# Kernel optimization log

Hardware: AMD Instinct MI355X
Metric: run time of the kernel (lower is better)

Reference implementation:

```python
import jax, jax.numpy as jnp
import numpy as np

N_NODES = 100000
N_EDGES = 1600000
D_IN = 256
D_OUT = 256


def _init_linear(key, out_f, in_f):
    # torch nn.Linear default: U(-1/sqrt(in_f), 1/sqrt(in_f))
    kw, kb = jax.random.split(key)
    bound = 1.0 / np.sqrt(in_f)
    W = jax.random.uniform(kw, (out_f, in_f), jnp.float32, -bound, bound)
    b = jax.random.uniform(kb, (out_f,), jnp.float32, -bound, bound)
    return W, b


def setup_inputs() -> dict:
    key = jax.random.key(0)
    ks = jax.random.split(key, 7)
    x = jax.random.normal(ks[0], (N_NODES, D_IN), jnp.float32)
    edge_index = jax.random.randint(ks[1], (2, N_EDGES), 0, N_NODES, jnp.int64)
    W1, b1 = _init_linear(ks[2], D_OUT, D_IN)
    W2, b2 = _init_linear(ks[3], D_OUT // 2, D_OUT)
    W3, b3 = _init_linear(ks[4], D_OUT // 2, D_OUT)
    Wd1, bd1 = _init_linear(ks[5], D_OUT, D_OUT)
    Wd2, bd2 = _init_linear(ks[6], 1, D_OUT)
    return {"x": x, "edge_index": edge_index,
            "W1": W1, "b1": b1, "W2": W2, "b2": b2, "W3": W3, "b3": b3,
            "Wd1": Wd1, "bd1": bd1, "Wd2": Wd2, "bd2": bd2}


def _l2norm(x):
    return x / jnp.linalg.norm(x, axis=-1, keepdims=True)


def reference(x, edge_index, W1, b1, W2, b2, W3, b3, Wd1, bd1, Wd2, bd2):
    src, dst = edge_index[0], edge_index[1]  # source_to_target flow
    x = jax.nn.relu(x @ W1.T + b1)           # [N, D_OUT]
    x = _l2norm(x)
    for _ in range(2):
        # sum-aggregate neighbor messages: scatter-add x[src] into dst
        nm = jax.ops.segment_sum(x[src], dst, num_segments=N_NODES)  # [N, D_OUT]
        x = jax.nn.relu(jnp.concatenate([x @ W2.T + b2, nm @ W3.T + b3], axis=-1))
        x = _l2norm(x)
    x = jax.nn.relu(x @ Wd1.T + bd1)
    return x @ Wd2.T + bd2                    # [N, 1]
```

## Files before the change

kernel.cpp:

```cpp
#include <hip/hip_runtime.h>
#include <math.h>


typedef _Float16 f16x8 __attribute__((ext_vector_type(8)));
typedef float    f32x16 __attribute__((ext_vector_type(16)));

constexpr int DIM = 256;
constexpr int BM  = 128;
constexpr int BK  = 32;
constexpr int SA  = 40;

__device__ __forceinline__ unsigned pk_hi2(float a, float b) {
    unsigned short ha = __builtin_bit_cast(unsigned short, (_Float16)a);
    unsigned short hb = __builtin_bit_cast(unsigned short, (_Float16)b);
    return (unsigned)ha | ((unsigned)hb << 16);
}
__device__ __forceinline__ unsigned pk_lo2(float a, float b) {
    _Float16 ha = (_Float16)a, hb = (_Float16)b;
    unsigned short la = __builtin_bit_cast(unsigned short, (_Float16)(a - (float)ha));
    unsigned short lb = __builtin_bit_cast(unsigned short, (_Float16)(b - (float)hb));
    return (unsigned)la | ((unsigned)lb << 16);
}
__device__ __forceinline__ unsigned pack_pair(float v) {
    _Float16 hi = (_Float16)v;
    _Float16 lo = (_Float16)(v - (float)hi);
    return (unsigned)__builtin_bit_cast(unsigned short, hi)
         | ((unsigned)__builtin_bit_cast(unsigned short, lo) << 16);
}

template <int AMODE, int EPI>
__device__ __forceinline__
void gemm_body(const void* __restrict__ Av,
               const float* __restrict__ WA, const float* __restrict__ WB,
               const float* __restrict__ bA, const float* __restrict__ bB,
               void* __restrict__ outv,
               const float* __restrict__ wd2, const float* __restrict__ bd2,
               float* __restrict__ out1, int M)
{
    __shared__ __align__(16) _Float16 smem[30720];
    _Float16* As_hi = smem;
    _Float16* As_lo = smem + 5120;
    _Float16* Ws_hi = smem + 10240;
    _Float16* Ws_lo = smem + 20480;

    const int tid = threadIdx.x;
    const int l31 = tid & 31;
    const int lh  = (tid >> 5) & 1;
    const int w   = tid >> 6;
    const int wr  = w >> 2;
    const int wc  = w & 3;
    const int bm0 = blockIdx.x * BM;

    const unsigned* Au = (const unsigned*)Av;
    const int srow = tid >> 2;
    const int sch  = (tid & 3) * 8;
    const int srw  = tid >> 1;
    const int scw  = (tid & 1) * 16;

    uint4 pa[2];
    auto fetchA = [&](int t) {
        const int k0 = t * BK;
        const int gr = bm0 + srow;
        if (gr < M) {
            pa[0] = *(const uint4*)&Au[(size_t)gr * 256 + k0 + sch];
            pa[1] = *(const uint4*)&Au[(size_t)gr * 256 + k0 + sch + 4];
        } else {
            pa[0] = uint4{0u,0u,0u,0u}; pa[1] = uint4{0u,0u,0u,0u};
        }
    };
    auto stageA = [&]() {
        uint4 hi, lo;
        if (AMODE == 0) {
            const float x0 = __builtin_bit_cast(float, pa[0].x);
            const float x1 = __builtin_bit_cast(float, pa[0].y);
            const float x2 = __builtin_bit_cast(float, pa[0].z);
            const float x3 = __builtin_bit_cast(float, pa[0].w);
            const float x4 = __builtin_bit_cast(float, pa[1].x);
            const float x5 = __builtin_bit_cast(float, pa[1].y);
            const float x6 = __builtin_bit_cast(float, pa[1].z);
            const float x7 = __builtin_bit_cast(float, pa[1].w);
            hi = uint4{pk_hi2(x0,x1), pk_hi2(x2,x3), pk_hi2(x4,x5), pk_hi2(x6,x7)};
            lo = uint4{pk_lo2(x0,x1), pk_lo2(x2,x3), pk_lo2(x4,x5), pk_lo2(x6,x7)};
        } else {
            hi = uint4{__builtin_amdgcn_perm(pa[0].y, pa[0].x, 0x05040100u),
                       __builtin_amdgcn_perm(pa[0].w, pa[0].z, 0x05040100u),
                       __builtin_amdgcn_perm(pa[1].y, pa[1].x, 0x05040100u),
                       __builtin_amdgcn_perm(pa[1].w, pa[1].z, 0x05040100u)};
            lo = uint4{__builtin_amdgcn_perm(pa[0].y, pa[0].x, 0x07060302u),
                       __builtin_amdgcn_perm(pa[0].w, pa[0].z, 0x07060302u),
                       __builtin_amdgcn_perm(pa[1].y, pa[1].x, 0x07060302u),
                       __builtin_amdgcn_perm(pa[1].w, pa[1].z, 0x07060302u)};
        }
        *(uint4*)&As_hi[srow * SA + sch] = hi;
        *(uint4*)&As_lo[srow * SA + sch] = lo;
    };
    auto stageW = [&](int t) {
        const int k0 = t * BK;
        const float* src = (srw < 128) ? &WA[(size_t)srw * 256]
                                       : &WB[(size_t)(srw - 128) * 256];
        const float4 w0 = *(const float4*)&src[k0 + scw];
        const float4 w1 = *(const float4*)&src[k0 + scw + 4];
        const float4 w2 = *(const float4*)&src[k0 + scw + 8];
        const float4 w3 = *(const float4*)&src[k0 + scw + 12];
        uint4 hi0{pk_hi2(w0.x,w0.y), pk_hi2(w0.z,w0.w), pk_hi2(w1.x,w1.y), pk_hi2(w1.z,w1.w)};
        uint4 hi1{pk_hi2(w2.x,w2.y), pk_hi2(w2.z,w2.w), pk_hi2(w3.x,w3.y), pk_hi2(w3.z,w3.w)};
        uint4 lo0{pk_lo2(w0.x,w0.y), pk_lo2(w0.z,w0.w), pk_lo2(w1.x,w1.y), pk_lo2(w1.z,w1.w)};
        uint4 lo1{pk_lo2(w2.x,w2.y), pk_lo2(w2.z,w2.w), pk_lo2(w3.x,w3.y), pk_lo2(w3.z,w3.w)};
        *(uint4*)&Ws_hi[srw * SA + scw]     = hi0;
        *(uint4*)&Ws_hi[srw * SA + scw + 8] = hi1;
        *(uint4*)&Ws_lo[srw * SA + scw]     = lo0;
        *(uint4*)&Ws_lo[srw * SA + scw + 8] = lo1;
    };

    f32x16 acc[2][2];
    #pragma unroll
    for (int tr = 0; tr < 2; ++tr)
        #pragma unroll
        for (int tc = 0; tc < 2; ++tc)
            #pragma unroll
            for (int i = 0; i < 16; ++i) acc[tr][tc][i] = 0.0f;

    fetchA(0);

    #pragma unroll 1
    for (int t = 0; t < DIM / BK; ++t) {
        stageA();
        stageW(t);
        __syncthreads();
        if (t < DIM / BK - 1) fetchA(t + 1);

        #pragma unroll
        for (int ks = 0; ks < 2; ++ks) {
            f16x8 ah[2], al[2], wh[2], wl[2];
            #pragma unroll
            for (int tr = 0; tr < 2; ++tr) {
                const int off = (wr * 64 + tr * 32 + l31) * SA + ks * 16 + lh * 8;
                ah[tr] = *(const f16x8*)&As_hi[off];
                al[tr] = *(const f16x8*)&As_lo[off];
            }
            #pragma unroll
            for (int tc = 0; tc < 2; ++tc) {
                const int off = (wc * 64 + tc * 32 + l31) * SA + ks * 16 + lh * 8;
                wh[tc] = *(const f16x8*)&Ws_hi[off];
                wl[tc] = *(const f16x8*)&Ws_lo[off];
            }
            #pragma unroll
            for (int tr = 0; tr < 2; ++tr)
                #pragma unroll
                for (int tc = 0; tc < 2; ++tc) {
                    acc[tr][tc] = __builtin_amdgcn_mfma_f32_32x32x16_f16(ah[tr], wh[tc], acc[tr][tc], 0, 0, 0);
                    acc[tr][tc] = __builtin_amdgcn_mfma_f32_32x32x16_f16(ah[tr], wl[tc], acc[tr][tc], 0, 0, 0);
                    acc[tr][tc] = __builtin_amdgcn_mfma_f32_32x32x16_f16(al[tr], wh[tc], acc[tr][tc], 0, 0, 0);
                }
        }
        __syncthreads();
    }


    if (EPI == 0) {
        float* z = (float*)outv;
        #pragma unroll
        for (int tr = 0; tr < 2; ++tr)
            #pragma unroll
            for (int i = 0; i < 16; ++i) {
                const int r  = wr * 64 + tr * 32 + 4 * lh + (i & 3) + 8 * (i >> 2);
                const int gr = bm0 + r;
                if (gr < M) {
                    #pragma unroll
                    for (int tc = 0; tc < 2; ++tc)
                        z[(size_t)gr * 256 + wc * 64 + tc * 32 + l31] = acc[tr][tc][i];
                }
            }
        return;
    }

    {
        float bias[2];
        #pragma unroll
        for (int tc = 0; tc < 2; ++tc) {
            const int col = wc * 64 + tc * 32 + l31;
            bias[tc] = (col < 128) ? bA[col] : bB[col - 128];
        }
        #pragma unroll
        for (int tr = 0; tr < 2; ++tr)
            #pragma unroll
            for (int tc = 0; tc < 2; ++tc)
                #pragma unroll
                for (int i = 0; i < 16; ++i)
                    acc[tr][tc][i] = fmaxf(acc[tr][tc][i] + bias[tc], 0.0f);
    }

    float* red = (float*)smem;

    if (EPI == 1) {
        #pragma unroll
        for (int tr = 0; tr < 2; ++tr)
            #pragma unroll
            for (int i = 0; i < 16; ++i) {
                float s = acc[tr][0][i] * acc[tr][0][i] + acc[tr][1][i] * acc[tr][1][i];
                #pragma unroll
                for (int m = 1; m < 32; m <<= 1) s += __shfl_xor(s, m);
                if (l31 == tr * 16 + i) {
                    const int r = wr * 64 + tr * 32 + 4 * lh + (i & 3) + 8 * (i >> 2);
                    red[r * 4 + wc] = s;
                }
            }
        __syncthreads();

        unsigned* hp = (unsigned*)outv;
        #pragma unroll
        for (int tr = 0; tr < 2; ++tr)
            #pragma unroll
            for (int i = 0; i < 16; ++i) {
                const int rl = wr * 64 + tr * 32 + 4 * lh + (i & 3) + 8 * (i >> 2);
                const float inv = 1.0f / sqrtf(red[rl * 4] + red[rl * 4 + 1] +
                                               red[rl * 4 + 2] + red[rl * 4 + 3]);
                const int gr = bm0 + rl;
                if (gr < M) {
                    #pragma unroll
                    for (int tc = 0; tc < 2; ++tc)
                        hp[(size_t)gr * 256 + wc * 64 + tc * 32 + l31] =
                            pack_pair(acc[tr][tc][i] * inv);
                }
            }
        return;
    }

    {
        float wv[2];
        #pragma unroll
        for (int tc = 0; tc < 2; ++tc) wv[tc] = wd2[wc * 64 + tc * 32 + l31];
        #pragma unroll
        for (int tr = 0; tr < 2; ++tr)
            #pragma unroll
            for (int i = 0; i < 16; ++i) {
                float s = acc[tr][0][i] * wv[0] + acc[tr][1][i] * wv[1];
                #pragma unroll
                for (int m = 1; m < 32; m <<= 1) s += __shfl_xor(s, m);
                if (l31 == tr * 16 + i) {
                    const int r = wr * 64 + tr * 32 + 4 * lh + (i & 3) + 8 * (i >> 2);
                    red[r * 4 + wc] = s;
                }
            }
        __syncthreads();
        if (tid < 128) {
            const int gr = bm0 + tid;
            if (gr < M)
                out1[gr] = red[tid * 4] + red[tid * 4 + 1] + red[tid * 4 + 2] +
                           red[tid * 4 + 3] + bd2[0];
        }
    }
}

__global__ __launch_bounds__(512, 4)
void gemm_l1(const void* __restrict__ Av,
             const float* __restrict__ WA, const float* __restrict__ WB,
             const float* __restrict__ bA, const float* __restrict__ bB,
             void* __restrict__ outv, int M, int gb,
             const int* __restrict__ ei, int E, int* __restrict__ cnt)
{
    if ((int)blockIdx.x < gb) {
        gemm_body<0, 1>(Av, WA, WB, bA, bB, outv, nullptr, nullptr, nullptr, M);
    } else {
        const int base = ((int)blockIdx.x - gb) * 2048 + threadIdx.x;
        #pragma unroll
        for (int k = 0; k < 4; ++k) {
            const int e = base + k * 512;
            if (e < E) atomicAdd(&cnt[ei[E + e]], 1);
        }
    }
}

template <int DO_FILL>
__global__ __launch_bounds__(512, 4)
void gemm_z(const void* __restrict__ Av,
            const float* __restrict__ WA, const float* __restrict__ WB,
            void* __restrict__ outv, int M, int gb,
            const int* __restrict__ ei, int E,
            int* __restrict__ cursor, int* __restrict__ esrc)
{
    if ((int)blockIdx.x < gb) {
        gemm_body<1, 0>(Av, WA, WB, nullptr, nullptr, outv, nullptr, nullptr, nullptr, M);
    } else if (DO_FILL) {
        const int base = ((int)blockIdx.x - gb) * 2048 + threadIdx.x;
        #pragma unroll
        for (int k = 0; k < 4; ++k) {
            const int e = base + k * 512;
            if (e < E) {
                int d = ei[E + e];
                int p = atomicAdd(&cursor[d], 1);
                esrc[p] = ei[e];
            }
        }
    }
}

__global__ __launch_bounds__(512, 4)
void gemm_head(const void* __restrict__ Av,
               const float* __restrict__ WA, const float* __restrict__ WB,
               const float* __restrict__ bA, const float* __restrict__ bB,
               const float* __restrict__ wd2, const float* __restrict__ bd2,
               float* __restrict__ out1, int M)
{
    gemm_body<1, 2>(Av, WA, WB, bA, bB, nullptr, wd2, bd2, out1, M);
}


__global__ void scan1_kernel(const int* __restrict__ cnt, int n,
                             int* __restrict__ rp, int* __restrict__ sums)
{
    __shared__ int sm[1024];
    const int tid = threadIdx.x;
    const int i = blockIdx.x * 1024 + tid;
    const int v = (i < n) ? cnt[i] : 0;
    sm[tid] = v;
    __syncthreads();
    for (int off = 1; off < 1024; off <<= 1) {
        int t = (tid >= off) ? sm[tid - off] : 0;
        __syncthreads();
        sm[tid] += t;
        __syncthreads();
    }
    if (i < n) rp[i] = sm[tid] - v;
    if (tid == 1023) sums[blockIdx.x] = sm[tid];
}

__global__ void scan2_kernel(int* __restrict__ sums, int n)
{
    __shared__ int sm[128];
    const int tid = threadIdx.x;
    const int v = (tid < n) ? sums[tid] : 0;
    sm[tid] = v;
    __syncthreads();
    for (int off = 1; off < 128; off <<= 1) {
        int t = (tid >= off) ? sm[tid - off] : 0;
        __syncthreads();
        sm[tid] += t;
        __syncthreads();
    }
    if (tid < n) sums[tid] = sm[tid] - v;
}

__global__ void scan3_kernel(int* __restrict__ rp, const int* __restrict__ sums,
                             int* __restrict__ cursor, int n, int E)
{
    int i = blockIdx.x * blockDim.x + threadIdx.x;
    if (i < n) {
        int v = rp[i] + sums[i >> 10];
        rp[i] = v;
        cursor[i] = v;
    }
    if (i == 0) rp[n] = E;
}

__global__ __launch_bounds__(256)
void fin_kernel(const float* __restrict__ z, const int* __restrict__ rp,
                const int* __restrict__ esrc,
                const float* __restrict__ b2, const float* __restrict__ b3,
                unsigned* __restrict__ hp, int M)
{
    const int v    = blockIdx.x * 4 + (threadIdx.x >> 6);
    const int lane = threadIdx.x & 63;
    if (v >= M) return;
    const int beg = rp[v], end = rp[v + 1];
    const int deg = end - beg;

    const float2 z1 = *(const float2*)&z[(size_t)v * DIM + lane * 2];
    const float2 c2 = *(const float2*)&b2[lane * 2];
    const float2 c3 = *(const float2*)&b3[lane * 2];

    const float* z2 = z + 128;
    float ax0 = 0.f, ay0 = 0.f, ax1 = 0.f, ay1 = 0.f;
    float ax2 = 0.f, ay2 = 0.f, ax3 = 0.f, ay3 = 0.f;

    for (int base = 0; base < deg; base += 64) {
        const int cnt = min(64, deg - base);
        int myidx = 0;
        if (lane < cnt) myidx = esrc[beg + base + lane];
        int j = 0;
        for (; j + 3 < cnt; j += 4) {
            const int s0 = __builtin_amdgcn_readlane(myidx, j);
            const int s1 = __builtin_amdgcn_readlane(myidx, j + 1);
            const int s2 = __builtin_amdgcn_readlane(myidx, j + 2);
            const int s3 = __builtin_amdgcn_readlane(myidx, j + 3);
            const float2 g0 = *(const float2*)&z2[(size_t)s0 * DIM + lane * 2];
            const float2 g1 = *(const float2*)&z2[(size_t)s1 * DIM + lane * 2];
            const float2 g2 = *(const float2*)&z2[(size_t)s2 * DIM + lane * 2];
            const float2 g3 = *(const float2*)&z2[(size_t)s3 * DIM + lane * 2];
            ax0 += g0.x; ay0 += g0.y;
            ax1 += g1.x; ay1 += g1.y;
            ax2 += g2.x; ay2 += g2.y;
            ax3 += g3.x; ay3 += g3.y;
        }
        for (; j < cnt; ++j) {
            const int s0 = __builtin_amdgcn_readlane(myidx, j);
            const float2 g0 = *(const float2*)&z2[(size_t)s0 * DIM + lane * 2];
            ax0 += g0.x; ay0 += g0.y;
        }
    }
    const float sx = (ax0 + ax1) + (ax2 + ax3);
    const float sy = (ay0 + ay1) + (ay2 + ay3);

    const float u1x = fmaxf(z1.x + c2.x, 0.f), u1y = fmaxf(z1.y + c2.y, 0.f);
    const float u2x = fmaxf(sx + c3.x, 0.f),  u2y = fmaxf(sy + c3.y, 0.f);

    float ss = u1x * u1x + u1y * u1y + u2x * u2x + u2y * u2y;
    #pragma unroll
    for (int off = 32; off > 0; off >>= 1) ss += __shfl_xor(ss, off);
    const float inv = 1.0f / sqrtf(ss);

    uint2 p1; p1.x = pack_pair(u1x * inv); p1.y = pack_pair(u1y * inv);
    uint2 p2; p2.x = pack_pair(u2x * inv); p2.y = pack_pair(u2y * inv);
    *(uint2*)&hp[(size_t)v * DIM + lane * 2]       = p1;
    *(uint2*)&hp[(size_t)v * DIM + 128 + lane * 2] = p2;
}


extern "C" void kernel_launch(void* const* d_in, const int* in_sizes, int n_in,
                              void* d_out, int out_size, void* d_ws, size_t ws_size,
                              hipStream_t stream)
{
    const float* x   = (const float*)d_in[0];
    const int*   ei  = (const int*)d_in[1];
    const float* W1  = (const float*)d_in[2];
    const float* b1  = (const float*)d_in[3];
    const float* W2  = (const float*)d_in[4];
    const float* b2  = (const float*)d_in[5];
    const float* W3  = (const float*)d_in[6];
    const float* b3  = (const float*)d_in[7];
    const float* Wd1 = (const float*)d_in[8];
    const float* bd1 = (const float*)d_in[9];
    const float* Wd2 = (const float*)d_in[10];
    const float* bd2 = (const float*)d_in[11];
    float* out = (float*)d_out;

    const int M = in_sizes[0] / DIM;
    const int E = in_sizes[1] / 2;

    unsigned* hp  = (unsigned*)d_ws;
    float*    z   = (float*)(hp + (size_t)M * DIM);
    int*   rp     = (int*)(z + (size_t)M * DIM);
    int*   cursor = rp + (M + 1);
    int*   esrc   = cursor + M;
    int*   sums   = esrc + E;

    hipMemsetAsync(cursor, 0, sizeof(int) * M, stream);

    const int gb  = (M + BM - 1) / BM;
    const int hb  = (E + 2047) / 2048;
    const int nb1 = (M + 1023) / 1024;
    const int fb  = (M + 3) / 4;

    gemm_l1<<<gb + hb, 512, 0, stream>>>(
        x, W1, W1 + 128 * DIM, b1, b1 + 128, hp, M, gb, ei, E, cursor);

    scan1_kernel<<<nb1, 1024, 0, stream>>>(cursor, M, rp, sums);
    scan2_kernel<<<1, 128, 0, stream>>>(sums, nb1);
    scan3_kernel<<<(M + 255) / 256, 256, 0, stream>>>(rp, sums, cursor, M, E);

    gemm_z<1><<<gb + hb, 512, 0, stream>>>(hp, W2, W3, z, M, gb, ei, E, cursor, esrc);
    fin_kernel<<<fb, 256, 0, stream>>>(z, rp, esrc, b2, b3, hp, M);

    gemm_z<0><<<gb, 512, 0, stream>>>(hp, W2, W3, z, M, gb, nullptr, 0, nullptr, nullptr);
    fin_kernel<<<fb, 256, 0, stream>>>(z, rp, esrc, b2, b3, hp, M);

    gemm_head<<<gb, 512, 0, stream>>>(
        hp, Wd1, Wd1 + 128 * DIM, bd1, bd1 + 128, Wd2, bd2, out, M);
}
```

Measured before the change: 748.1 us.

## Replace tiled GEMMs for z and head with weight-resident streaming GEMM

The z and head GEMMs now use a new kernel in which each block loads a 64-column slice of the fp32 weights once into shared memory as hi/lo fp16 pairs. The A rows are then streamed directly from global memory into MFMA registers, with no shared-memory staging or per-K-tile syncthreads. The z output is transposed through shared memory so it can be written as coalesced float4 stores. The head epilogue splits its final dot product across four column groups and combines them with atomicAdd into an output that is zeroed beforehand. The trade-offs are redundant A reads across the four column groups, atomics on the output, and an extra memset.

```diff
diff --git a/kernel.cpp b/kernel.cpp
--- a/kernel.cpp
+++ b/kernel.cpp
@@ -9,6 +9,7 @@
 constexpr int BM  = 128;
 constexpr int BK  = 32;
 constexpr int SA  = 40;
+constexpr int WS  = 264;
 
 __device__ __forceinline__ unsigned pk_hi2(float a, float b) {
     unsigned short ha = __builtin_bit_cast(unsigned short, (_Float16)a);
@@ -28,14 +29,11 @@
          | ((unsigned)__builtin_bit_cast(unsigned short, lo) << 16);
 }
 
-template <int AMODE, int EPI>
 __device__ __forceinline__
-void gemm_body(const void* __restrict__ Av,
-               const float* __restrict__ WA, const float* __restrict__ WB,
-               const float* __restrict__ bA, const float* __restrict__ bB,
-               void* __restrict__ outv,
-               const float* __restrict__ wd2, const float* __restrict__ bd2,
-               float* __restrict__ out1, int M)
+void gemm_body_l1(const void* __restrict__ Av,
+                  const float* __restrict__ WA, const float* __restrict__ WB,
+                  const float* __restrict__ bA, const float* __restrict__ bB,
+                  void* __restrict__ outv, int M)
 {
     __shared__ __align__(16) _Float16 smem[30720];
     _Float16* As_hi = smem;
@@ -69,28 +67,16 @@
         }
     };
     auto stageA = [&]() {
-        uint4 hi, lo;
-        if (AMODE == 0) {
-            const float x0 = __builtin_bit_cast(float, pa[0].x);
-            const float x1 = __builtin_bit_cast(float, pa[0].y);
-            const float x2 = __builtin_bit_cast(float, pa[0].z);
-            const float x3 = __builtin_bit_cast(float, pa[0].w);
-            const float x4 = __builtin_bit_cast(float, pa[1].x);
-            const float x5 = __builtin_bit_cast(float, pa[1].y);
-            const float x6 = __builtin_bit_cast(float, pa[1].z);
-            const float x7 = __builtin_bit_cast(float, pa[1].w);
-            hi = uint4{pk_hi2(x0,x1), pk_hi2(x2,x3), pk_hi2(x4,x5), pk_hi2(x6,x7)};
-            lo = uint4{pk_lo2(x0,x1), pk_lo2(x2,x3), pk_lo2(x4,x5), pk_lo2(x6,x7)};
-        } else {
-            hi = uint4{__builtin_amdgcn_perm(pa[0].y, pa[0].x, 0x05040100u),
-                       __builtin_amdgcn_perm(pa[0].w, pa[0].z, 0x05040100u),
-                       __builtin_amdgcn_perm(pa[1].y, pa[1].x, 0x05040100u),
-                       __builtin_amdgcn_perm(pa[1].w, pa[1].z, 0x05040100u)};
-            lo = uint4{__builtin_amdgcn_perm(pa[0].y, pa[0].x, 0x07060302u),
-                       __builtin_amdgcn_perm(pa[0].w, pa[0].z, 0x07060302u),
-                       __builtin_amdgcn_perm(pa[1].y, pa[1].x, 0x07060302u),
-                       __builtin_amdgcn_perm(pa[1].w, pa[1].z, 0x07060302u)};
-        }
+        const float x0 = __builtin_bit_cast(float, pa[0].x);
+        const float x1 = __builtin_bit_cast(float, pa[0].y);
+        const float x2 = __builtin_bit_cast(float, pa[0].z);
+        const float x3 = __builtin_bit_cast(float, pa[0].w);
+        const float x4 = __builtin_bit_cast(float, pa[1].x);
+        const float x5 = __builtin_bit_cast(float, pa[1].y);
+        const float x6 = __builtin_bit_cast(float, pa[1].z);
+        const float x7 = __builtin_bit_cast(float, pa[1].w);
+        uint4 hi{pk_hi2(x0,x1), pk_hi2(x2,x3), pk_hi2(x4,x5), pk_hi2(x6,x7)};
+        uint4 lo{pk_lo2(x0,x1), pk_lo2(x2,x3), pk_lo2(x4,x5), pk_lo2(x6,x7)};
         *(uint4*)&As_hi[srow * SA + sch] = hi;
         *(uint4*)&As_lo[srow * SA + sch] = lo;
     };
@@ -156,24 +142,6 @@
         __syncthreads();
     }
 
-
-    if (EPI == 0) {
-        float* z = (float*)outv;
-        #pragma unroll
-        for (int tr = 0; tr < 2; ++tr)
-            #pragma unroll
-            for (int i = 0; i < 16; ++i) {
-                const int r  = wr * 64 + tr * 32 + 4 * lh + (i & 3) + 8 * (i >> 2);
-                const int gr = bm0 + r;
-                if (gr < M) {
-                    #pragma unroll
-                    for (int tc = 0; tc < 2; ++tc)
-                        z[(size_t)gr * 256 + wc * 64 + tc * 32 + l31] = acc[tr][tc][i];
-                }
-            }
-        return;
-    }
-
     {
         float bias[2];
         #pragma unroll
@@ -191,65 +159,36 @@
     }
 
     float* red = (float*)smem;
-
-    if (EPI == 1) {
-        #pragma unroll
-        for (int tr = 0; tr < 2; ++tr)
-            #pragma unroll
-            for (int i = 0; i < 16; ++i) {
-                float s = acc[tr][0][i] * acc[tr][0][i] + acc[tr][1][i] * acc[tr][1][i];
+    #pragma unroll
+    for (int tr = 0; tr < 2; ++tr)
+        #pragma unroll
+        for (int i = 0; i < 16; ++i) {
+            float s = acc[tr][0][i] * acc[tr][0][i] + acc[tr][1][i] * acc[tr][1][i];
+            #pragma unroll
+            for (int m = 1; m < 32; m <<= 1) s += __shfl_xor(s, m);
+            if (l31 == tr * 16 + i) {
+                const int r = wr * 64 + tr * 32 + 4 * lh + (i & 3) + 8 * (i >> 2);
+                red[r * 4 + wc] = s;
+            }
+        }
+    __syncthreads();
+
+    unsigned* hp = (unsigned*)outv;
+    #pragma unroll
+    for (int tr = 0; tr < 2; ++tr)
+        #pragma unroll
+        for (int i = 0; i < 16; ++i) {
+            const int rl = wr * 64 + tr * 32 + 4 * lh + (i & 3) + 8 * (i >> 2);
+            const float inv = 1.0f / sqrtf(red[rl * 4] + red[rl * 4 + 1] +
+                                           red[rl * 4 + 2] + red[rl * 4 + 3]);
+            const int gr = bm0 + rl;
+            if (gr < M) {
                 #pragma unroll
-                for (int m = 1; m < 32; m <<= 1) s += __shfl_xor(s, m);
-                if (l31 == tr * 16 + i) {
-                    const int r = wr * 64 + tr * 32 + 4 * lh + (i & 3) + 8 * (i >> 2);
-                    red[r * 4 + wc] = s;
-                }
+                for (int tc = 0; tc < 2; ++tc)
+                    hp[(size_t)gr * 256 + wc * 64 + tc * 32 + l31] =
+                        pack_pair(acc[tr][tc][i] * inv);
             }
-        __syncthreads();
-
-        unsigned* hp = (unsigned*)outv;
-        #pragma unroll
-        for (int tr = 0; tr < 2; ++tr)
-            #pragma unroll
-            for (int i = 0; i < 16; ++i) {
-                const int rl = wr * 64 + tr * 32 + 4 * lh + (i & 3) + 8 * (i >> 2);
-                const float inv = 1.0f / sqrtf(red[rl * 4] + red[rl * 4 + 1] +
-                                               red[rl * 4 + 2] + red[rl * 4 + 3]);
-                const int gr = bm0 + rl;
-                if (gr < M) {
-                    #pragma unroll
-                    for (int tc = 0; tc < 2; ++tc)
-                        hp[(size_t)gr * 256 + wc * 64 + tc * 32 + l31] =
-                            pack_pair(acc[tr][tc][i] * inv);
-                }
-            }
-        return;
-    }
-
-    {
-        float wv[2];
-        #pragma unroll
-        for (int tc = 0; tc < 2; ++tc) wv[tc] = wd2[wc * 64 + tc * 32 + l31];
-        #pragma unroll
-        for (int tr = 0; tr < 2; ++tr)
-            #pragma unroll
-            for (int i = 0; i < 16; ++i) {
-                float s = acc[tr][0][i] * wv[0] + acc[tr][1][i] * wv[1];
-                #pragma unroll
-                for (int m = 1; m < 32; m <<= 1) s += __shfl_xor(s, m);
-                if (l31 == tr * 16 + i) {
-                    const int r = wr * 64 + tr * 32 + 4 * lh + (i & 3) + 8 * (i >> 2);
-                    red[r * 4 + wc] = s;
-                }
-            }
-        __syncthreads();
-        if (tid < 128) {
-            const int gr = bm0 + tid;
-            if (gr < M)
-                out1[gr] = red[tid * 4] + red[tid * 4 + 1] + red[tid * 4 + 2] +
-                           red[tid * 4 + 3] + bd2[0];
-        }
-    }
+        }
 }
 
 __global__ __launch_bounds__(512, 4)
@@ -260,7 +199,7 @@
              const int* __restrict__ ei, int E, int* __restrict__ cnt)
 {
     if ((int)blockIdx.x < gb) {
-        gemm_body<0, 1>(Av, WA, WB, bA, bB, outv, nullptr, nullptr, nullptr, M);
+        gemm_body_l1(Av, WA, WB, bA, bB, outv, M);
     } else {
         const int base = ((int)blockIdx.x - gb) * 2048 + threadIdx.x;
         #pragma unroll
@@ -271,18 +210,136 @@
     }
 }
 
-template <int DO_FILL>
+template <int EPI>
+__device__ __forceinline__
+void gemm_stream_body(const unsigned* __restrict__ Au,
+                      const float* __restrict__ WA, const float* __restrict__ WB,
+                      const float* __restrict__ b256,
+                      float* __restrict__ zout,
+                      const float* __restrict__ wd2, const float* __restrict__ bd2,
+                      float* __restrict__ out1, int M)
+{
+    __shared__ __align__(16) _Float16 smem[33792];
+    _Float16* Wh = smem;
+    _Float16* Wl = smem + 16896;
+
+    const int tid = threadIdx.x;
+    const int rb  = (int)blockIdx.x >> 2;
+    const int cg  = (int)blockIdx.x & 3;
+
+    {
+        const int nl = tid >> 3;
+        const int kb = (tid & 7) * 32;
+        const int ng = cg * 64 + nl;
+        const float* src = (ng < 128) ? &WA[(size_t)ng * 256]
+                                      : &WB[(size_t)(ng - 128) * 256];
+        #pragma unroll
+        for (int j = 0; j < 4; ++j) {
+            const float4 a = *(const float4*)&src[kb + j * 8];
+            const float4 b = *(const float4*)&src[kb + j * 8 + 4];
+            uint4 hi{pk_hi2(a.x,a.y), pk_hi2(a.z,a.w), pk_hi2(b.x,b.y), pk_hi2(b.z,b.w)};
+            uint4 lo{pk_lo2(a.x,a.y), pk_lo2(a.z,a.w), pk_lo2(b.x,b.y), pk_lo2(b.z,b.w)};
+            *(uint4*)&Wh[nl * WS + kb + j * 8] = hi;
+            *(uint4*)&Wl[nl * WS + kb + j * 8] = lo;
+        }
+    }
+    __syncthreads();
+
+    const int lane = tid & 63;
+    const int l31  = lane & 31;
+    const int lh   = lane >> 5;
+    const int w    = tid >> 6;
+    const int row0 = rb * 256 + w * 32 + l31;
+    const unsigned* arow = Au + (size_t)min(row0, M - 1) * 256;
+
+    f32x16 acc[2];
+    #pragma unroll
+    for (int tc = 0; tc < 2; ++tc)
+        #pragma unroll
+        for (int i = 0; i < 16; ++i) acc[tc][i] = 0.0f;
+
+    #pragma unroll 4
+    for (int t = 0; t < 16; ++t) {
+        const int ku = t * 16 + lh * 8;
+        const uint4 p0 = *(const uint4*)&arow[ku];
+        const uint4 p1 = *(const uint4*)&arow[ku + 4];
+        uint4 h{__builtin_amdgcn_perm(p0.y, p0.x, 0x05040100u),
+                __builtin_amdgcn_perm(p0.w, p0.z, 0x05040100u),
+                __builtin_amdgcn_perm(p1.y, p1.x, 0x05040100u),
+                __builtin_amdgcn_perm(p1.w, p1.z, 0x05040100u)};
+        uint4 l{__builtin_amdgcn_perm(p0.y, p0.x, 0x07060302u),
+                __builtin_amdgcn_perm(p0.w, p0.z, 0x07060302u),
+                __builtin_amdgcn_perm(p1.y, p1.x, 0x07060302u),
+                __builtin_amdgcn_perm(p1.w, p1.z, 0x07060302u)};
+        const f16x8 ah = __builtin_bit_cast(f16x8, h);
+        const f16x8 al = __builtin_bit_cast(f16x8, l);
+        #pragma unroll
+        for (int tc = 0; tc < 2; ++tc) {
+            const int off = (tc * 32 + l31) * WS + t * 16 + lh * 8;
+            const f16x8 wh = *(const f16x8*)&Wh[off];
+            const f16x8 wl = *(const f16x8*)&Wl[off];
+            acc[tc] = __builtin_amdgcn_mfma_f32_32x32x16_f16(ah, wh, acc[tc], 0, 0, 0);
+            acc[tc] = __builtin_amdgcn_mfma_f32_32x32x16_f16(ah, wl, acc[tc], 0, 0, 0);
+            acc[tc] = __builtin_amdgcn_mfma_f32_32x32x16_f16(al, wh, acc[tc], 0, 0, 0);
+        }
+    }
+
+
+    if (EPI == 0) {
+        __syncthreads();
+        float* scr = (float*)smem + w * 2112;
+        #pragma unroll
+        for (int tc = 0; tc < 2; ++tc)
+            #pragma unroll
+            for (int i = 0; i < 16; ++i) {
+                const int r32 = (i & 3) + 8 * (i >> 2) + 4 * lh;
+                scr[r32 * 66 + tc * 32 + l31] = acc[tc][i];
+            }
+        __syncthreads();
+        const int rr = lane >> 4;
+        const int cc = (lane & 15) * 4;
+        #pragma unroll
+        for (int i = 0; i < 8; ++i) {
+            const int r32 = i * 4 + rr;
+            const int gr  = rb * 256 + w * 32 + r32;
+            const float4 v = *(const float4*)&scr[r32 * 66 + cc];
+            if (gr < M)
+                *(float4*)&zout[(size_t)gr * 256 + cg * 64 + cc] = v;
+        }
+        return;
+    }
+
+    {
+        float bias[2], wv[2];
+        #pragma unroll
+        for (int tc = 0; tc < 2; ++tc) {
+            const int col = cg * 64 + tc * 32 + l31;
+            bias[tc] = b256[col];
+            wv[tc]   = wd2[col];
+        }
+        const float bdv = (cg == 0) ? bd2[0] : 0.0f;
+        #pragma unroll
+        for (int i = 0; i < 16; ++i) {
+            float s = fmaxf(acc[0][i] + bias[0], 0.0f) * wv[0]
+                    + fmaxf(acc[1][i] + bias[1], 0.0f) * wv[1];
+            #pragma unroll
+            for (int m = 1; m < 32; m <<= 1) s += __shfl_xor(s, m);
+            const int r32 = (i & 3) + 8 * (i >> 2) + 4 * lh;
+            const int gr  = rb * 256 + w * 32 + r32;
+            if (l31 == 0 && gr < M) atomicAdd(&out1[gr], s + bdv);
+        }
+    }
+}
+
 __global__ __launch_bounds__(512, 4)
-void gemm_z(const void* __restrict__ Av,
-            const float* __restrict__ WA, const float* __restrict__ WB,
-            void* __restrict__ outv, int M, int gb,
-            const int* __restrict__ ei, int E,
-            int* __restrict__ cursor, int* __restrict__ esrc)
-{
-    if ((int)blockIdx.x < gb) {
-        gemm_body<1, 0>(Av, WA, WB, nullptr, nullptr, outv, nullptr, nullptr, nullptr, M);
-    } else if (DO_FILL) {
-        const int base = ((int)blockIdx.x - gb) * 2048 + threadIdx.x;
+void gemm_zs(const unsigned* __restrict__ Au,
+             const float* __restrict__ WA, const float* __restrict__ WB,
+             float* __restrict__ zout, int M, int nstream,
+             const int* __restrict__ ei, int E,
+             int* __restrict__ cursor, int* __restrict__ esrc)
+{
+    if ((int)blockIdx.x >= nstream) {
+        const int base = ((int)blockIdx.x - nstream) * 2048 + threadIdx.x;
         #pragma unroll
         for (int k = 0; k < 4; ++k) {
             const int e = base + k * 512;
@@ -292,17 +349,19 @@
                 esrc[p] = ei[e];
             }
         }
-    }
+        return;
+    }
+    gemm_stream_body<0>(Au, WA, WB, nullptr, zout, nullptr, nullptr, nullptr, M);
 }
 
 __global__ __launch_bounds__(512, 4)
-void gemm_head(const void* __restrict__ Av,
-               const float* __restrict__ WA, const float* __restrict__ WB,
-               const float* __restrict__ bA, const float* __restrict__ bB,
-               const float* __restrict__ wd2, const float* __restrict__ bd2,
-               float* __restrict__ out1, int M)
-{
-    gemm_body<1, 2>(Av, WA, WB, bA, bB, nullptr, wd2, bd2, out1, M);
+void gemm_hs(const unsigned* __restrict__ Au,
+             const float* __restrict__ WA, const float* __restrict__ WB,
+             const float* __restrict__ b256,
+             const float* __restrict__ wd2, const float* __restrict__ bd2,
+             float* __restrict__ out1, int M)
+{
+    gemm_stream_body<2>(Au, WA, WB, b256, nullptr, wd2, bd2, out1, M);
 }
 
 
@@ -445,9 +504,11 @@
     int*   sums   = esrc + E;
 
     hipMemsetAsync(cursor, 0, sizeof(int) * M, stream);
+    hipMemsetAsync(out, 0, sizeof(float) * out_size, stream);
 
     const int gb  = (M + BM - 1) / BM;
     const int hb  = (E + 2047) / 2048;
+    const int sb  = ((M + 255) / 256) * 4;
     const int nb1 = (M + 1023) / 1024;
     const int fb  = (M + 3) / 4;
 
@@ -458,12 +519,12 @@
     scan2_kernel<<<1, 128, 0, stream>>>(sums, nb1);
     scan3_kernel<<<(M + 255) / 256, 256, 0, stream>>>(rp, sums, cursor, M, E);
 
-    gemm_z<1><<<gb + hb, 512, 0, stream>>>(hp, W2, W3, z, M, gb, ei, E, cursor, esrc);
+    gemm_zs<<<sb + hb, 512, 0, stream>>>(hp, W2, W3, z, M, sb, ei, E, cursor, esrc);
     fin_kernel<<<fb, 256, 0, stream>>>(z, rp, esrc, b2, b3, hp, M);
 
-    gemm_z<0><<<gb, 512, 0, stream>>>(hp, W2, W3, z, M, gb, nullptr, 0, nullptr, nullptr);
+    gemm_zs<<<sb, 512, 0, stream>>>(hp, W2, W3, z, M, sb, nullptr, 0, nullptr, nullptr);
     fin_kernel<<<fb, 256, 0, stream>>>(z, rp, esrc, b2, b3, hp, M);
 
-    gemm_head<<<gb, 512, 0, stream>>>(
-        hp, Wd1, Wd1 + 128 * DIM, bd1, bd1 + 128, Wd2, bd2, out, M);
-}
+    gemm_hs<<<sb, 512, 0, stream>>>(
+        hp, Wd1, Wd1 + 128 * DIM, bd1, Wd2, bd2, out, M);
+}
```

Result: slower. 895.6 us (+19.7%).

## Split z into contiguous halves and stage GEMM epilogue stores through LDS

Applied to the files above, without the earlier changes.

The GEMM output z is split into two separate [M,128] arrays, so the gather in fin_kernel reads contiguous 512-byte rows of the neighbor half instead of strided half-rows of a 256-wide array. The GEMM epilogues (EPI 0 and EPI 1) now write accumulators into a padded shared-memory scratch in 32-row chunks and then emit coalesced 8-byte-per-lane row stores, instead of scattered 4-byte stores in MFMA fragment order. This adds extra __syncthreads and LDS round trips per chunk. The EPI 1 reduction buffer moves to a separate smem offset so it does not clash with the scratch.

```diff
diff --git a/kernel.cpp b/kernel.cpp
--- a/kernel.cpp
+++ b/kernel.cpp
@@ -33,7 +33,8 @@
 void gemm_body(const void* __restrict__ Av,
                const float* __restrict__ WA, const float* __restrict__ WB,
                const float* __restrict__ bA, const float* __restrict__ bB,
-               void* __restrict__ outv,
+               float* __restrict__ z1p, float* __restrict__ z2p,
+               void* __restrict__ hpv,
                const float* __restrict__ wd2, const float* __restrict__ bd2,
                float* __restrict__ out1, int M)
 {
@@ -46,6 +47,7 @@
     const int tid = threadIdx.x;
     const int l31 = tid & 31;
     const int lh  = (tid >> 5) & 1;
+    const int lane = tid & 63;
     const int w   = tid >> 6;
     const int wr  = w >> 2;
     const int wc  = w & 3;
@@ -158,19 +160,33 @@
 
 
     if (EPI == 0) {
-        float* z = (float*)outv;
-        #pragma unroll
-        for (int tr = 0; tr < 2; ++tr)
-            #pragma unroll
-            for (int i = 0; i < 16; ++i) {
-                const int r  = wr * 64 + tr * 32 + 4 * lh + (i & 3) + 8 * (i >> 2);
-                const int gr = bm0 + r;
-                if (gr < M) {
+        float* scr = (float*)smem;
+        #pragma unroll 1
+        for (int c = 0; c < 4; ++c) {
+            __syncthreads();
+            if (wr == (c >> 1)) {
+                const int tr = c & 1;
+                #pragma unroll
+                for (int i = 0; i < 16; ++i) {
+                    const int r32 = 4 * lh + (i & 3) + 8 * (i >> 2);
                     #pragma unroll
                     for (int tc = 0; tc < 2; ++tc)
-                        z[(size_t)gr * 256 + wc * 64 + tc * 32 + l31] = acc[tr][tc][i];
-                }
-            }
+                        scr[r32 * 260 + wc * 64 + tc * 32 + l31] = acc[tr][tc][i];
+                }
+            }
+            __syncthreads();
+            #pragma unroll
+            for (int rr = 0; rr < 4; ++rr) {
+                const int r32 = w * 4 + rr;
+                const int gr  = bm0 + c * 32 + r32;
+                if (gr < M) {
+                    const float2 v1 = *(const float2*)&scr[r32 * 260 + lane * 2];
+                    const float2 v2 = *(const float2*)&scr[r32 * 260 + 128 + lane * 2];
+                    *(float2*)&z1p[(size_t)gr * 128 + lane * 2] = v1;
+                    *(float2*)&z2p[(size_t)gr * 128 + lane * 2] = v2;
+                }
+            }
+        }
         return;
     }
 
@@ -190,9 +206,8 @@
                     acc[tr][tc][i] = fmaxf(acc[tr][tc][i] + bias[tc], 0.0f);
     }
 
-    float* red = (float*)smem;
-
     if (EPI == 1) {
+        float* red = (float*)(smem + 20000);
         #pragma unroll
         for (int tr = 0; tr < 2; ++tr)
             #pragma unroll
@@ -207,26 +222,43 @@
             }
         __syncthreads();
 
-        unsigned* hp = (unsigned*)outv;
-        #pragma unroll
-        for (int tr = 0; tr < 2; ++tr)
-            #pragma unroll
-            for (int i = 0; i < 16; ++i) {
-                const int rl = wr * 64 + tr * 32 + 4 * lh + (i & 3) + 8 * (i >> 2);
-                const float inv = 1.0f / sqrtf(red[rl * 4] + red[rl * 4 + 1] +
-                                               red[rl * 4 + 2] + red[rl * 4 + 3]);
-                const int gr = bm0 + rl;
-                if (gr < M) {
+        unsigned* hp  = (unsigned*)hpv;
+        unsigned* scr = (unsigned*)smem;
+        #pragma unroll 1
+        for (int c = 0; c < 4; ++c) {
+            __syncthreads();
+            if (wr == (c >> 1)) {
+                const int tr = c & 1;
+                #pragma unroll
+                for (int i = 0; i < 16; ++i) {
+                    const int r32 = 4 * lh + (i & 3) + 8 * (i >> 2);
+                    const int rl  = c * 32 + r32;
+                    const float inv = 1.0f / sqrtf(red[rl * 4] + red[rl * 4 + 1] +
+                                                   red[rl * 4 + 2] + red[rl * 4 + 3]);
                     #pragma unroll
                     for (int tc = 0; tc < 2; ++tc)
-                        hp[(size_t)gr * 256 + wc * 64 + tc * 32 + l31] =
+                        scr[r32 * 260 + wc * 64 + tc * 32 + l31] =
                             pack_pair(acc[tr][tc][i] * inv);
                 }
             }
+            __syncthreads();
+            #pragma unroll
+            for (int rr = 0; rr < 4; ++rr) {
+                const int r32 = w * 4 + rr;
+                const int gr  = bm0 + c * 32 + r32;
+                if (gr < M) {
+                    const uint2 v1 = *(const uint2*)&scr[r32 * 260 + lane * 2];
+                    const uint2 v2 = *(const uint2*)&scr[r32 * 260 + 128 + lane * 2];
+                    *(uint2*)&hp[(size_t)gr * 256 + lane * 2]       = v1;
+                    *(uint2*)&hp[(size_t)gr * 256 + 128 + lane * 2] = v2;
+                }
+            }
+        }
         return;
     }
 
     {
+        float* red = (float*)smem;
         float wv[2];
         #pragma unroll
         for (int tc = 0; tc < 2; ++tc) wv[tc] = wd2[wc * 64 + tc * 32 + l31];
@@ -256,11 +288,12 @@
 void gemm_l1(const void* __restrict__ Av,
              const float* __restrict__ WA, const float* __restrict__ WB,
              const float* __restrict__ bA, const float* __restrict__ bB,
-             void* __restrict__ outv, int M, int gb,
+             void* __restrict__ hpv, int M, int gb,
              const int* __restrict__ ei, int E, int* __restrict__ cnt)
 {
     if ((int)blockIdx.x < gb) {
-        gemm_body<0, 1>(Av, WA, WB, bA, bB, outv, nullptr, nullptr, nullptr, M);
+        gemm_body<0, 1>(Av, WA, WB, bA, bB, nullptr, nullptr, hpv,
+                        nullptr, nullptr, nullptr, M);
     } else {
         const int base = ((int)blockIdx.x - gb) * 2048 + threadIdx.x;
         #pragma unroll
@@ -275,12 +308,13 @@
 __global__ __launch_bounds__(512, 4)
 void gemm_z(const void* __restrict__ Av,
             const float* __restrict__ WA, const float* __restrict__ WB,
-            void* __restrict__ outv, int M, int gb,
+            float* __restrict__ z1p, float* __restrict__ z2p, int M, int gb,
             const int* __restrict__ ei, int E,
             int* __restrict__ cursor, int* __restrict__ esrc)
 {
     if ((int)blockIdx.x < gb) {
-        gemm_body<1, 0>(Av, WA, WB, nullptr, nullptr, outv, nullptr, nullptr, nullptr, M);
+        gemm_body<1, 0>(Av, WA, WB, nullptr, nullptr, z1p, z2p, nullptr,
+                        nullptr, nullptr, nullptr, M);
     } else if (DO_FILL) {
         const int base = ((int)blockIdx.x - gb) * 2048 + threadIdx.x;
         #pragma unroll
@@ -302,7 +336,8 @@
                const float* __restrict__ wd2, const float* __restrict__ bd2,
                float* __restrict__ out1, int M)
 {
-    gemm_body<1, 2>(Av, WA, WB, bA, bB, nullptr, wd2, bd2, out1, M);
+    gemm_body<1, 2>(Av, WA, WB, bA, bB, nullptr, nullptr, nullptr,
+                    wd2, bd2, out1, M);
 }
 
 
@@ -354,8 +389,8 @@
 }
 
 __global__ __launch_bounds__(256)
-void fin_kernel(const float* __restrict__ z, const int* __restrict__ rp,
-                const int* __restrict__ esrc,
+void fin_kernel(const float* __restrict__ z1p, const float* __restrict__ z2p,
+                const int* __restrict__ rp, const int* __restrict__ esrc,
                 const float* __restrict__ b2, const float* __restrict__ b3,
                 unsigned* __restrict__ hp, int M)
 {
@@ -365,11 +400,10 @@
     const int beg = rp[v], end = rp[v + 1];
     const int deg = end - beg;
 
-    const float2 z1 = *(const float2*)&z[(size_t)v * DIM + lane * 2];
+    const float2 z1 = *(const float2*)&z1p[(size_t)v * 128 + lane * 2];
     const float2 c2 = *(const float2*)&b2[lane * 2];
     const float2 c3 = *(const float2*)&b3[lane * 2];
 
-    const float* z2 = z + 128;
     float ax0 = 0.f, ay0 = 0.f, ax1 = 0.f, ay1 = 0.f;
     float ax2 = 0.f, ay2 = 0.f, ax3 = 0.f, ay3 = 0.f;
 
@@ -383,10 +417,10 @@
             const int s1 = __builtin_amdgcn_readlane(myidx, j + 1);
             const int s2 = __builtin_amdgcn_readlane(myidx, j + 2);
             const int s3 = __builtin_amdgcn_readlane(myidx, j + 3);
-            const float2 g0 = *(const float2*)&z2[(size_t)s0 * DIM + lane * 2];
-            const float2 g1 = *(const float2*)&z2[(size_t)s1 * DIM + lane * 2];
-            const float2 g2 = *(const float2*)&z2[(size_t)s2 * DIM + lane * 2];
-            const float2 g3 = *(const float2*)&z2[(size_t)s3 * DIM + lane * 2];
+            const float2 g0 = *(const float2*)&z2p[(size_t)s0 * 128 + lane * 2];
+            const float2 g1 = *(const float2*)&z2p[(size_t)s1 * 128 + lane * 2];
+            const float2 g2 = *(const float2*)&z2p[(size_t)s2 * 128 + lane * 2];
+            const float2 g3 = *(const float2*)&z2p[(size_t)s3 * 128 + lane * 2];
             ax0 += g0.x; ay0 += g0.y;
             ax1 += g1.x; ay1 += g1.y;
             ax2 += g2.x; ay2 += g2.y;
@@ -394,7 +428,7 @@
         }
         for (; j < cnt; ++j) {
             const int s0 = __builtin_amdgcn_readlane(myidx, j);
-            const float2 g0 = *(const float2*)&z2[(size_t)s0 * DIM + lane * 2];
+            const float2 g0 = *(const float2*)&z2p[(size_t)s0 * 128 + lane * 2];
             ax0 += g0.x; ay0 += g0.y;
         }
     }
@@ -438,8 +472,9 @@
     const int E = in_sizes[1] / 2;
 
     unsigned* hp  = (unsigned*)d_ws;
-    float*    z   = (float*)(hp + (size_t)M * DIM);
-    int*   rp     = (int*)(z + (size_t)M * DIM);
+    float*    z1p = (float*)(hp + (size_t)M * DIM);
+    float*    z2p = z1p + (size_t)M * 128;
+    int*   rp     = (int*)(z2p + (size_t)M * 128);
     int*   cursor = rp + (M + 1);
     int*   esrc   = cursor + M;
     int*   sums   = esrc + E;
@@ -458,11 +493,11 @@
     scan2_kernel<<<1, 128, 0, stream>>>(sums, nb1);
     scan3_kernel<<<(M + 255) / 256, 256, 0, stream>>>(rp, sums, cursor, M, E);
 
-    gemm_z<1><<<gb + hb, 512, 0, stream>>>(hp, W2, W3, z, M, gb, ei, E, cursor, esrc);
-    fin_kernel<<<fb, 256, 0, stream>>>(z, rp, esrc, b2, b3, hp, M);
-
-    gemm_z<0><<<gb, 512, 0, stream>>>(hp, W2, W3, z, M, gb, nullptr, 0, nullptr, nullptr);
-    fin_kernel<<<fb, 256, 0, stream>>>(z, rp, esrc, b2, b3, hp, M);
+    gemm_z<1><<<gb + hb, 512, 0, stream>>>(hp, W2, W3, z1p, z2p, M, gb, ei, E, cursor, esrc);
+    fin_kernel<<<fb, 256, 0, stream>>>(z1p, z2p, rp, esrc, b2, b3, hp, M);
+
+    gemm_z<0><<<gb, 512, 0, stream>>>(hp, W2, W3, z1p, z2p, M, gb, nullptr, 0, nullptr, nullptr);
+    fin_kernel<<<fb, 256, 0, stream>>>(z1p, z2p, rp, esrc, b2, b3, hp, M);
 
     gemm_head<<<gb, 512, 0, stream>>>(
         hp, Wd1, Wd1 + 128 * DIM, bd1, bd1 + 128, Wd2, bd2, out, M);
```

New measurement: 1.241 ms. 65.9% more time.
